# Performance work log

Hardware: AMD Instinct MI355X
Metric: run time of the kernel (lower is better)

Reference implementation:

```python
import jax, jax.numpy as jnp
import numpy as np

N = 50000      # nodes
E = 600000     # edges
G = 512        # graphs in batch
F_IN = 128     # input node features
H = 128        # hidden size (both layers)
PH = 128       # pool/classifier hidden size


def setup_inputs() -> dict:
    key = jax.random.key(0)
    ks = jax.random.split(key, 12)
    def lin(k, fi, fo):
        return (jax.random.normal(k, (fi, fo), jnp.float32) / np.sqrt(fi)).astype(jnp.float32)
    return {
        "x": jax.random.normal(ks[0], (N, F_IN), jnp.float32),
        "edge_index": jax.random.randint(ks[1], (2, E), 0, N),
        "batch": jnp.sort(jax.random.randint(ks[2], (N,), 0, G)),
        "W1": lin(ks[3], F_IN, H), "b1": jnp.zeros((H,), jnp.float32),
        "ln1_g": jnp.ones((H,), jnp.float32), "ln1_b": jnp.zeros((H,), jnp.float32),
        "W2": lin(ks[4], H, H), "b2": jnp.zeros((H,), jnp.float32),
        "ln2_g": jnp.ones((H,), jnp.float32), "ln2_b": jnp.zeros((H,), jnp.float32),
        "gate_w1": lin(ks[5], H, PH), "gate_b1": jnp.zeros((PH,), jnp.float32),
        "gate_w2": lin(ks[6], PH, 1), "gate_b2": jnp.zeros((1,), jnp.float32),
        "cls_w1": lin(ks[7], H, PH), "cls_b1": jnp.zeros((PH,), jnp.float32),
        "cls_w2": lin(ks[8], PH, 2), "cls_b2": jnp.zeros((2,), jnp.float32),
    }


def _layer_norm(h, g, b):
    m = h.mean(-1, keepdims=True)
    v = ((h - m) ** 2).mean(-1, keepdims=True)
    return (h - m) * jax.lax.rsqrt(v + 1e-5) * g + b


def _gcn(x, src, dst, norm, W, b):
    # GCNConv: x' = D^{-1/2} (A+I) D^{-1/2} (x W) + b
    h = x @ W
    out = jax.ops.segment_sum(h[src] * norm[:, None], dst, num_segments=N)
    return out + b


def reference(x, edge_index, batch, W1, b1, ln1_g, ln1_b, W2, b2, ln2_g, ln2_b,
              gate_w1, gate_b1, gate_w2, gate_b2, cls_w1, cls_b1, cls_w2, cls_b2):
    loops = jnp.arange(N, dtype=edge_index.dtype)
    src = jnp.concatenate([edge_index[0], loops])
    dst = jnp.concatenate([edge_index[1], loops])
    deg = jax.ops.segment_sum(jnp.ones_like(src, dtype=x.dtype), dst, num_segments=N)
    dinv = jnp.where(deg > 0, jax.lax.rsqrt(jnp.maximum(deg, 1e-12)), 0.0)
    norm = dinv[src] * dinv[dst]  # [(E+N)]

    h = jax.nn.relu(_layer_norm(_gcn(x, src, dst, norm, W1, b1), ln1_g, ln1_b))
    h = jax.nn.relu(_layer_norm(_gcn(h, src, dst, norm, W2, b2), ln2_g, ln2_b))

    # GlobalAttention pooling: gate MLP -> scatter softmax over graphs -> weighted sum
    gate = (jax.nn.relu(h @ gate_w1 + gate_b1) @ gate_w2 + gate_b2)[:, 0]  # [N]
    gmax = jax.ops.segment_max(gate, batch, num_segments=G)
    a = jnp.exp(gate - gmax[batch])
    denom = jax.ops.segment_sum(a, batch, num_segments=G)
    alpha = a / denom[batch]
    pooled = jax.ops.segment_sum(alpha[:, None] * h, batch, num_segments=G)  # [G, H]

    logits = jax.nn.relu(pooled @ cls_w1 + cls_b1) @ cls_w2 + cls_b2  # [G, 2]
    return logits
```

## Files before the change

kernel.cpp:

```cpp
#include <hip/hip_runtime.h>
#include <hip/hip_bf16.h>

typedef short s8v __attribute__((ext_vector_type(8)));
typedef float f4v __attribute__((ext_vector_type(4)));

#define LDA 136

__device__ __forceinline__ unsigned short f2bf(float f) {
  unsigned int u = __builtin_bit_cast(unsigned int, f);
  unsigned int r = u + 0x7fffu + ((u >> 16) & 1u);
  return (unsigned short)(r >> 16);
}
__device__ __forceinline__ float bf2f(unsigned short s) {
  return __builtin_bit_cast(float, ((unsigned int)s) << 16);
}
__device__ __forceinline__ float bflo(unsigned int v) {
  return __builtin_bit_cast(float, (unsigned int)(v << 16));
}
__device__ __forceinline__ float bfhi(unsigned int v) {
  return __builtin_bit_cast(float, (unsigned int)(v & 0xffff0000u));
}
__device__ __forceinline__ unsigned int packbf(float a, float b) {
  return (unsigned int)f2bf(a) | ((unsigned int)f2bf(b) << 16);
}

__device__ __forceinline__ int lower_bound_i(const int* a, int n, int key) {
  int lo = 0, hi = n;
  while (lo < hi) { int mid = (lo + hi) >> 1; if (a[mid] < key) lo = mid + 1; else hi = mid; }
  return lo;
}

__device__ __forceinline__ void gather_sum(
    int i, int sub, const int* __restrict__ offs, const int* __restrict__ col,
    const uint4* __restrict__ hu, float acc[8]) {
  uint4 hv = hu[(size_t)i * 16 + sub];
  acc[0] = bflo(hv.x); acc[1] = bfhi(hv.x);
  acc[2] = bflo(hv.y); acc[3] = bfhi(hv.y);
  acc[4] = bflo(hv.z); acc[5] = bfhi(hv.z);
  acc[6] = bflo(hv.w); acc[7] = bfhi(hv.w);
  int b0 = offs[i], b1 = offs[i + 1];
  int e = b0;
  for (; e + 4 <= b1; e += 4) {
    int s0 = col[e], s1 = col[e + 1], s2 = col[e + 2], s3 = col[e + 3];
    uint4 h0 = hu[(size_t)s0 * 16 + sub];
    uint4 h1 = hu[(size_t)s1 * 16 + sub];
    uint4 h2 = hu[(size_t)s2 * 16 + sub];
    uint4 h3 = hu[(size_t)s3 * 16 + sub];
    acc[0] += bflo(h0.x) + bflo(h1.x) + bflo(h2.x) + bflo(h3.x);
    acc[1] += bfhi(h0.x) + bfhi(h1.x) + bfhi(h2.x) + bfhi(h3.x);
    acc[2] += bflo(h0.y) + bflo(h1.y) + bflo(h2.y) + bflo(h3.y);
    acc[3] += bfhi(h0.y) + bfhi(h1.y) + bfhi(h2.y) + bfhi(h3.y);
    acc[4] += bflo(h0.z) + bflo(h1.z) + bflo(h2.z) + bflo(h3.z);
    acc[5] += bfhi(h0.z) + bfhi(h1.z) + bfhi(h2.z) + bfhi(h3.z);
    acc[6] += bflo(h0.w) + bflo(h1.w) + bflo(h2.w) + bflo(h3.w);
    acc[7] += bfhi(h0.w) + bfhi(h1.w) + bfhi(h2.w) + bfhi(h3.w);
  }
  for (; e < b1; ++e) {
    int s0 = col[e];
    uint4 h0 = hu[(size_t)s0 * 16 + sub];
    acc[0] += bflo(h0.x); acc[1] += bfhi(h0.x);
    acc[2] += bflo(h0.y); acc[3] += bfhi(h0.y);
    acc[4] += bflo(h0.z); acc[5] += bfhi(h0.z);
    acc[6] += bflo(h0.w); acc[7] += bfhi(h0.w);
  }
}

__device__ __forceinline__ uint4 ln_relu_pack(
    float v[8], int sub, const float* __restrict__ gam, const float* __restrict__ bet) {
  float s = 0.f, q = 0.f;
#pragma unroll
  for (int j = 0; j < 8; ++j) { s += v[j]; q += v[j] * v[j]; }
#pragma unroll
  for (int o = 1; o < 16; o <<= 1) {
    s += __shfl_xor(s, o);
    q += __shfl_xor(q, o);
  }
  float m = s * (1.0f / 128.0f);
  float var = q * (1.0f / 128.0f) - m * m;
  float rs = rsqrtf(var + 1e-5f);
  float4 g0 = reinterpret_cast<const float4*>(gam)[sub * 2];
  float4 g1 = reinterpret_cast<const float4*>(gam)[sub * 2 + 1];
  float4 e0 = reinterpret_cast<const float4*>(bet)[sub * 2];
  float4 e1 = reinterpret_cast<const float4*>(bet)[sub * 2 + 1];
  uint4 ov;
  ov.x = packbf(fmaxf((v[0] - m) * rs * g0.x + e0.x, 0.f), fmaxf((v[1] - m) * rs * g0.y + e0.y, 0.f));
  ov.y = packbf(fmaxf((v[2] - m) * rs * g0.z + e0.z, 0.f), fmaxf((v[3] - m) * rs * g0.w + e0.w, 0.f));
  ov.z = packbf(fmaxf((v[4] - m) * rs * g1.x + e1.x, 0.f), fmaxf((v[5] - m) * rs * g1.y + e1.y, 0.f));
  ov.w = packbf(fmaxf((v[6] - m) * rs * g1.z + e1.z, 0.f), fmaxf((v[7] - m) * rs * g1.w + e1.w, 0.f));
  return ov;
}

__device__ __forceinline__ void scale_bias(
    float acc[8], float di, int sub, const float* __restrict__ bias, float v[8]) {
  float4 b0v = reinterpret_cast<const float4*>(bias)[sub * 2];
  float4 b1v = reinterpret_cast<const float4*>(bias)[sub * 2 + 1];
  v[0] = acc[0] * di + b0v.x; v[1] = acc[1] * di + b0v.y;
  v[2] = acc[2] * di + b0v.z; v[3] = acc[3] * di + b0v.w;
  v[4] = acc[4] * di + b1v.x; v[5] = acc[5] * di + b1v.y;
  v[6] = acc[6] * di + b1v.z; v[7] = acc[7] * di + b1v.w;
}

__global__ __launch_bounds__(256) void pack_zero(
    const float* __restrict__ Wa, const float* __restrict__ Wb, const float* __restrict__ Wc,
    unsigned short* __restrict__ P, unsigned int* __restrict__ deg, int n) {
  int bid = blockIdx.x;
  if (bid >= 384) {
    int i = (bid - 384) * 256 + threadIdx.x;
    if (i < n) deg[i] = 0u;
    return;
  }
  int gidx = bid * 256 + threadIdx.x;
  int which = gidx >> 15;
  int idx = gidx & 32767;
  const float* W = (which == 0) ? Wa : (which == 1) ? Wb : Wc;
  int j = idx & 15;
  int lane = (idx >> 4) & 63;
  int t = (idx >> 10) & 7;
  int c = (idx >> 13) & 3;
  int k = c * 32 + (lane >> 4) * 8 + (j & 7);
  int nn = t * 16 + (lane & 15);
  float f = W[k * 128 + nn];
  unsigned short hi = f2bf(f);
  unsigned short outv = (j < 8) ? hi : f2bf(f - bf2f(hi));
  P[gidx] = outv;
}

__global__ void accum_deg(const int* __restrict__ dst, unsigned int* __restrict__ deg, int E) {
  int e = blockIdx.x * blockDim.x + threadIdx.x;
  if (e < E) atomicAdd(&deg[dst[e]], 1u);
}

__global__ __launch_bounds__(256) void scanA(const unsigned int* __restrict__ deg,
                                             int* __restrict__ offs, int* __restrict__ partial,
                                             float* __restrict__ dinv, int n) {
  __shared__ int sh[256];
  int t = threadIdx.x;
  int i = blockIdx.x * 256 + t;
  int v = (i < n) ? (int)deg[i] : 0;
  if (i < n) dinv[i] = rsqrtf((float)(deg[i] + 1u));
  sh[t] = v;
  __syncthreads();
  for (int o = 1; o < 256; o <<= 1) {
    int add = (t >= o) ? sh[t - o] : 0;
    __syncthreads();
    sh[t] += add;
    __syncthreads();
  }
  if (i < n) offs[i] = sh[t] - v;
  if (t == 255) partial[blockIdx.x] = sh[255];
}

__global__ __launch_bounds__(256) void scanC(int* __restrict__ offs, const int* __restrict__ partial,
                                             int* __restrict__ cursor, int n, int E) {
  __shared__ int red[256];
  int bid = blockIdx.x;
  int t = threadIdx.x;
  int s = 0;
  for (int j = t; j < bid; j += 256) s += partial[j];
  red[t] = s;
  __syncthreads();
#pragma unroll
  for (int o = 128; o > 0; o >>= 1) {
    if (t < o) red[t] += red[t + o];
    __syncthreads();
  }
  int pre = red[0];
  int i = bid * 256 + t;
  if (i < n) {
    int o = offs[i] + pre;
    offs[i] = o;
    cursor[i] = o;
  }
  if (i == 0) offs[n] = E;
}

__global__ __launch_bounds__(256) void gemm1_scatter(
    const float* __restrict__ in, const unsigned short* __restrict__ P,
    unsigned short* __restrict__ out, int n,
    const int* __restrict__ src, const int* __restrict__ dst,
    int* __restrict__ cursor, int* __restrict__ col,
    const float* __restrict__ dinv, int E, int gemmBlocks) {
  if ((int)blockIdx.x >= gemmBlocks) {
    int e = ((int)blockIdx.x - gemmBlocks) * 256 + threadIdx.x;
    if (e < E) {
      int d = dst[e];
      int slot = atomicAdd(&cursor[d], 1);
      col[slot] = src[e];
    }
    return;
  }
  int tid = threadIdx.x;
  int wave = tid >> 6, lane = tid & 63;
  int quad = lane >> 4, c16 = lane & 15;
  int base = blockIdx.x * 64 + wave * 16;
  int m = base + c16;

  f4v acc[8];
#pragma unroll
  for (int t = 0; t < 8; ++t) acc[t] = (f4v){0.f, 0.f, 0.f, 0.f};

  for (int c = 0; c < 4; ++c) {
    s8v ah, al;
    float v[8];
    if (m < n) {
      const float4* xp = reinterpret_cast<const float4*>(in + (size_t)m * 128 + c * 32 + quad * 8);
      float4 v0 = xp[0], v1 = xp[1];
      v[0] = v0.x; v[1] = v0.y; v[2] = v0.z; v[3] = v0.w;
      v[4] = v1.x; v[5] = v1.y; v[6] = v1.z; v[7] = v1.w;
    } else {
#pragma unroll
      for (int j = 0; j < 8; ++j) v[j] = 0.f;
    }
#pragma unroll
    for (int j = 0; j < 8; ++j) {
      unsigned short h = f2bf(v[j]);
      ah[j] = (short)h;
      al[j] = (short)f2bf(v[j] - bf2f(h));
    }
#pragma unroll
    for (int t = 0; t < 8; ++t) {
      const s8v* bp = reinterpret_cast<const s8v*>(&P[((c * 8 + t) * 64 + lane) * 16]);
      s8v bh = bp[0], bl = bp[1];
      acc[t] = __builtin_amdgcn_mfma_f32_16x16x32_bf16(ah, bh, acc[t], 0, 0, 0);
      acc[t] = __builtin_amdgcn_mfma_f32_16x16x32_bf16(ah, bl, acc[t], 0, 0, 0);
      acc[t] = __builtin_amdgcn_mfma_f32_16x16x32_bf16(al, bh, acc[t], 0, 0, 0);
    }
  }
  float dv[4];
#pragma unroll
  for (int r = 0; r < 4; ++r) {
    int mm = base + quad * 4 + r;
    dv[r] = (mm < n) ? dinv[mm] : 0.f;
  }
#pragma unroll
  for (int t = 0; t < 8; ++t)
#pragma unroll
    for (int r = 0; r < 4; ++r) {
      int mm = base + quad * 4 + r;
      if (mm < n) out[(size_t)mm * 128 + t * 16 + c16] = f2bf(acc[t][r] * dv[r]);
    }
}

__global__ __launch_bounds__(256) void gather_gemm(
    const int* __restrict__ offs, const int* __restrict__ col,
    const float* __restrict__ dinv, const unsigned short* __restrict__ h,
    const float* __restrict__ bias, const float* __restrict__ gam,
    const float* __restrict__ bet, const unsigned short* __restrict__ P,
    unsigned short* __restrict__ out, int n) {
  __shared__ unsigned short A[64 * LDA];
  int tid = threadIdx.x;
  int wave = tid >> 6, lane = tid & 63;
  int grp = lane >> 4, sub = lane & 15;
  const uint4* hu = reinterpret_cast<const uint4*>(h);
  int blk = blockIdx.x * 64;
  for (int it = 0; it < 4; ++it) {
    int li = it * 16 + wave * 4 + grp;
    int i = blk + li;
    uint4 ov;
    if (i < n) {
      float acc[8], v[8];
      gather_sum(i, sub, offs, col, hu, acc);
      scale_bias(acc, dinv[i], sub, bias, v);
      ov = ln_relu_pack(v, sub, gam, bet);
    } else {
      ov = make_uint4(0u, 0u, 0u, 0u);
    }
    *reinterpret_cast<uint4*>(&A[li * LDA + sub * 8]) = ov;
  }
  __syncthreads();
  int quad = lane >> 4, c16 = lane & 15;
  f4v acc[8];
#pragma unroll
  for (int t = 0; t < 8; ++t) acc[t] = (f4v){0.f, 0.f, 0.f, 0.f};
  int liA = wave * 16 + c16;
  for (int c = 0; c < 4; ++c) {
    s8v ah = *reinterpret_cast<const s8v*>(&A[liA * LDA + c * 32 + quad * 8]);
#pragma unroll
    for (int t = 0; t < 8; ++t) {
      const s8v* bp = reinterpret_cast<const s8v*>(&P[((c * 8 + t) * 64 + lane) * 16]);
      s8v bh = bp[0], bl = bp[1];
      acc[t] = __builtin_amdgcn_mfma_f32_16x16x32_bf16(ah, bh, acc[t], 0, 0, 0);
      acc[t] = __builtin_amdgcn_mfma_f32_16x16x32_bf16(ah, bl, acc[t], 0, 0, 0);
    }
  }
  float dv[4];
#pragma unroll
  for (int r = 0; r < 4; ++r) {
    int mm = blk + wave * 16 + quad * 4 + r;
    dv[r] = (mm < n) ? dinv[mm] : 0.f;
  }
#pragma unroll
  for (int t = 0; t < 8; ++t)
#pragma unroll
    for (int r = 0; r < 4; ++r) {
      int mm = blk + wave * 16 + quad * 4 + r;
      if (mm < n) out[(size_t)mm * 128 + t * 16 + c16] = f2bf(acc[t][r] * dv[r]);
    }
}

__global__ __launch_bounds__(256) void gather_gate(
    const int* __restrict__ offs, const int* __restrict__ col,
    const float* __restrict__ dinv, const unsigned short* __restrict__ h,
    const float* __restrict__ bias, const float* __restrict__ gam,
    const float* __restrict__ bet, const unsigned short* __restrict__ P,
    const float* __restrict__ gb1, const float* __restrict__ gw2,
    const float* __restrict__ gb2, unsigned short* __restrict__ hout,
    float* __restrict__ gate, int n) {
  __shared__ unsigned short A[64 * LDA];
  int tid = threadIdx.x;
  int wave = tid >> 6, lane = tid & 63;
  int grp = lane >> 4, sub = lane & 15;
  const uint4* hu = reinterpret_cast<const uint4*>(h);
  int blk = blockIdx.x * 64;
  for (int it = 0; it < 4; ++it) {
    int li = it * 16 + wave * 4 + grp;
    int i = blk + li;
    uint4 ov;
    if (i < n) {
      float acc[8], v[8];
      gather_sum(i, sub, offs, col, hu, acc);
      scale_bias(acc, dinv[i], sub, bias, v);
      ov = ln_relu_pack(v, sub, gam, bet);
      reinterpret_cast<uint4*>(hout)[(size_t)i * 16 + sub] = ov;
    } else {
      ov = make_uint4(0u, 0u, 0u, 0u);
    }
    *reinterpret_cast<uint4*>(&A[li * LDA + sub * 8]) = ov;
  }
  __syncthreads();
  int quad = lane >> 4, c16 = lane & 15;
  f4v acc[8];
#pragma unroll
  for (int t = 0; t < 8; ++t) acc[t] = (f4v){0.f, 0.f, 0.f, 0.f};
  int liA = wave * 16 + c16;
  for (int c = 0; c < 4; ++c) {
    s8v ah = *reinterpret_cast<const s8v*>(&A[liA * LDA + c * 32 + quad * 8]);
#pragma unroll
    for (int t = 0; t < 8; ++t) {
      const s8v* bp = reinterpret_cast<const s8v*>(&P[((c * 8 + t) * 64 + lane) * 16]);
      s8v bh = bp[0], bl = bp[1];
      acc[t] = __builtin_amdgcn_mfma_f32_16x16x32_bf16(ah, bh, acc[t], 0, 0, 0);
      acc[t] = __builtin_amdgcn_mfma_f32_16x16x32_bf16(ah, bl, acc[t], 0, 0, 0);
    }
  }
  float bv[8], g2[8];
#pragma unroll
  for (int t = 0; t < 8; ++t) {
    bv[t] = gb1[t * 16 + c16];
    g2[t] = gw2[t * 16 + c16];
  }
  float gb2v = gb2[0];
#pragma unroll
  for (int r = 0; r < 4; ++r) {
    float p = 0.f;
#pragma unroll
    for (int t = 0; t < 8; ++t)
      p += fmaxf(acc[t][r] + bv[t], 0.f) * g2[t];
#pragma unroll
    for (int o = 1; o < 16; o <<= 1) p += __shfl_xor(p, o);
    int mm = blk + wave * 16 + quad * 4 + r;
    if (c16 == 0 && mm < n) gate[mm] = p + gb2v;
  }
}

__global__ __launch_bounds__(256) void pool_cls(
    float* __restrict__ gate, const unsigned short* __restrict__ h,
    const int* __restrict__ batch,
    const float* __restrict__ w1, const float* __restrict__ b1,
    const float* __restrict__ w2, const float* __restrict__ b2,
    float* __restrict__ out, int n) {
  int g = blockIdx.x;
  int tid = threadIdx.x;
  __shared__ float red[256];
  __shared__ float red2[256];
  __shared__ float p[128];
  __shared__ float r[128];
  int lo = lower_bound_i(batch, n, g);
  int hi = lower_bound_i(batch, n, g + 1);
  if (lo >= hi) {
    if (tid < 128) p[tid] = 0.0f;
  } else {
    float m = -3.0e38f;
    for (int i = lo + tid; i < hi; i += 256) m = fmaxf(m, gate[i]);
    red[tid] = m;
    __syncthreads();
#pragma unroll
    for (int o = 128; o > 0; o >>= 1) {
      if (tid < o) red[tid] = fmaxf(red[tid], red[tid + o]);
      __syncthreads();
    }
    m = red[0];
    __syncthreads();
    float s = 0.0f;
    for (int i = lo + tid; i < hi; i += 256) {
      float e = __expf(gate[i] - m);
      gate[i] = e;
      s += e;
    }
    red[tid] = s;
    __syncthreads();
#pragma unroll
    for (int o = 128; o > 0; o >>= 1) {
      if (tid < o) red[tid] += red[tid + o];
      __syncthreads();
    }
    float inv = 1.0f / red[0];
    __syncthreads();
    const unsigned int* hu = reinterpret_cast<const unsigned int*>(h);
    int j = tid & 63, rgp = tid >> 6;
    float a0 = 0.f, a1 = 0.f;
    int i = lo + rgp;
    for (; i + 4 < hi; i += 8) {
      unsigned int p0 = hu[(size_t)i * 64 + j];
      unsigned int p1 = hu[(size_t)(i + 4) * 64 + j];
      float w0 = gate[i], w1v = gate[i + 4];
      a0 += bflo(p0) * w0 + bflo(p1) * w1v;
      a1 += bfhi(p0) * w0 + bfhi(p1) * w1v;
    }
    if (i < hi) {
      unsigned int p0 = hu[(size_t)i * 64 + j];
      float w0 = gate[i];
      a0 += bflo(p0) * w0;
      a1 += bfhi(p0) * w0;
    }
    red[tid] = a0;
    red2[tid] = a1;
    __syncthreads();
    if (tid < 64) {
      p[2 * tid]     = (red[tid] + red[tid + 64] + red[tid + 128] + red[tid + 192]) * inv;
      p[2 * tid + 1] = (red2[tid] + red2[tid + 64] + red2[tid + 128] + red2[tid + 192]) * inv;
    }
  }
  __syncthreads();
  int j = tid & 127, half = tid >> 7;
  float acc = 0.0f;
#pragma unroll 8
  for (int k = half * 64; k < half * 64 + 64; ++k)
    acc = fmaf(p[k], w1[k * 128 + j], acc);
  red[tid] = acc;
  __syncthreads();
  if (tid < 128) r[tid] = fmaxf(red[tid] + red[tid + 128] + b1[tid], 0.0f);
  __syncthreads();
  if (tid < 2) {
    float a = 0.0f;
    for (int k = 0; k < 128; ++k) a = fmaf(r[k], w2[k * 2 + tid], a);
    out[g * 2 + tid] = a + b2[tid];
  }
}

static inline size_t alup(size_t x) { return (x + 255) & ~(size_t)255; }

extern "C" void kernel_launch(void* const* d_in, const int* in_sizes, int n_in,
                              void* d_out, int out_size, void* d_ws, size_t ws_size,
                              hipStream_t stream) {
  const float* x    = (const float*)d_in[0];
  const int*   ei   = (const int*)d_in[1];
  const int*   bat  = (const int*)d_in[2];
  const float* W1   = (const float*)d_in[3];
  const float* b1   = (const float*)d_in[4];
  const float* ln1g = (const float*)d_in[5];
  const float* ln1b = (const float*)d_in[6];
  const float* W2   = (const float*)d_in[7];
  const float* b2   = (const float*)d_in[8];
  const float* ln2g = (const float*)d_in[9];
  const float* ln2b = (const float*)d_in[10];
  const float* gw1  = (const float*)d_in[11];
  const float* gb1  = (const float*)d_in[12];
  const float* gw2  = (const float*)d_in[13];
  const float* gb2  = (const float*)d_in[14];
  const float* cw1  = (const float*)d_in[15];
  const float* cb1  = (const float*)d_in[16];
  const float* cw2  = (const float*)d_in[17];
  const float* cb2  = (const float*)d_in[18];

  const int N = in_sizes[2];
  const int E = in_sizes[1] / 2;
  const int G = out_size / 2;
  const int* src = ei;
  const int* dst = ei + E;

  int nb256 = (N + 255) / 256;
  int eb256 = (E + 255) / 256;
  int mfmaB = (N + 63) / 64;

  char* base = (char*)d_ws;
  unsigned int* deg = (unsigned int*)base; base += alup((size_t)N * 4);
  float* dinv = (float*)base;              base += alup((size_t)N * 4);
  int* offs = (int*)base;                  base += alup((size_t)(N + 1) * 4);
  int* cursor = (int*)base;                base += alup((size_t)N * 4);
  int* partial = (int*)base;               base += alup((size_t)nb256 * 4);
  int* col = (int*)base;                   base += alup((size_t)E * 4);
  unsigned short* pW = (unsigned short*)base; base += alup((size_t)3 * 32768 * 2);
  unsigned short* hbuf = (unsigned short*)base;  base += alup((size_t)N * 128 * 2);
  unsigned short* hbuf2 = (unsigned short*)base; base += alup((size_t)N * 128 * 2);
  unsigned short* hout = (unsigned short*)base;  base += alup((size_t)N * 128 * 2);
  float* gate = (float*)base;              base += alup((size_t)N * 4);

  unsigned short* pW1 = pW;
  unsigned short* pW2 = pW + 32768;
  unsigned short* pG1 = pW + 65536;

  float* out = (float*)d_out;

  pack_zero<<<384 + nb256, 256, 0, stream>>>(W1, W2, gw1, pW, deg, N);
  accum_deg<<<eb256, 256, 0, stream>>>(dst, deg, E);
  scanA<<<nb256, 256, 0, stream>>>(deg, offs, partial, dinv, N);
  scanC<<<nb256, 256, 0, stream>>>(offs, partial, cursor, N, E);
  gemm1_scatter<<<mfmaB + eb256, 256, 0, stream>>>(x, pW1, hbuf, N,
                                                   src, dst, cursor, col, dinv, E, mfmaB);
  gather_gemm<<<mfmaB, 256, 0, stream>>>(offs, col, dinv, hbuf, b1, ln1g, ln1b,
                                         pW2, hbuf2, N);
  gather_gate<<<mfmaB, 256, 0, stream>>>(offs, col, dinv, hbuf2, b2, ln2g, ln2b,
                                         pG1, gb1, gw2, gb2, hout, gate, N);
  pool_cls<<<G, 256, 0, stream>>>(gate, hout, bat, cw1, cb1, cw2, cb2, out, N);
}
```

Measured before the change: 272.3 us.

## Build CSR via two-level bucketed radix sort with LDS atomics

Replaces the global-atomic degree count, two-kernel scan and global-atomic scatter with a two-level counting sort: coarse 256-node buckets are histogrammed in shared memory, scanned in a single block, scattered as packed (local dst, src) words, then a per-bucket kernel builds the fine offsets, dinv and col using LDS atomics. Because dinv is no longer available when the first GEMM runs, the source-side normalisation moves from the GEMM epilogues into the gather loop, which now loads dinv per neighbour. This cuts kernel launches and contended global atomics. In exchange it adds an extra pass over the edges, uses a 16-bit src packing that only holds for fewer than 65536 nodes, and sizes buckets for at most 256×256 nodes. The single-block scan limits parallelism.

```diff
diff --git a/kernel.cpp b/kernel.cpp
--- a/kernel.cpp
+++ b/kernel.cpp
@@ -30,14 +30,15 @@
   return lo;
 }
 
-__device__ __forceinline__ void gather_sum(
+__device__ __forceinline__ float gather_node(
     int i, int sub, const int* __restrict__ offs, const int* __restrict__ col,
-    const uint4* __restrict__ hu, float acc[8]) {
+    const float* __restrict__ dinv, const uint4* __restrict__ hu, float acc[8]) {
+  float di = dinv[i];
   uint4 hv = hu[(size_t)i * 16 + sub];
-  acc[0] = bflo(hv.x); acc[1] = bfhi(hv.x);
-  acc[2] = bflo(hv.y); acc[3] = bfhi(hv.y);
-  acc[4] = bflo(hv.z); acc[5] = bfhi(hv.z);
-  acc[6] = bflo(hv.w); acc[7] = bfhi(hv.w);
+  acc[0] = bflo(hv.x) * di; acc[1] = bfhi(hv.x) * di;
+  acc[2] = bflo(hv.y) * di; acc[3] = bfhi(hv.y) * di;
+  acc[4] = bflo(hv.z) * di; acc[5] = bfhi(hv.z) * di;
+  acc[6] = bflo(hv.w) * di; acc[7] = bfhi(hv.w) * di;
   int b0 = offs[i], b1 = offs[i + 1];
   int e = b0;
   for (; e + 4 <= b1; e += 4) {
@@ -46,23 +47,26 @@
     uint4 h1 = hu[(size_t)s1 * 16 + sub];
     uint4 h2 = hu[(size_t)s2 * 16 + sub];
     uint4 h3 = hu[(size_t)s3 * 16 + sub];
-    acc[0] += bflo(h0.x) + bflo(h1.x) + bflo(h2.x) + bflo(h3.x);
-    acc[1] += bfhi(h0.x) + bfhi(h1.x) + bfhi(h2.x) + bfhi(h3.x);
-    acc[2] += bflo(h0.y) + bflo(h1.y) + bflo(h2.y) + bflo(h3.y);
-    acc[3] += bfhi(h0.y) + bfhi(h1.y) + bfhi(h2.y) + bfhi(h3.y);
-    acc[4] += bflo(h0.z) + bflo(h1.z) + bflo(h2.z) + bflo(h3.z);
-    acc[5] += bfhi(h0.z) + bfhi(h1.z) + bfhi(h2.z) + bfhi(h3.z);
-    acc[6] += bflo(h0.w) + bflo(h1.w) + bflo(h2.w) + bflo(h3.w);
-    acc[7] += bfhi(h0.w) + bfhi(h1.w) + bfhi(h2.w) + bfhi(h3.w);
+    float n0 = dinv[s0], n1 = dinv[s1], n2 = dinv[s2], n3 = dinv[s3];
+    acc[0] += bflo(h0.x) * n0 + bflo(h1.x) * n1 + bflo(h2.x) * n2 + bflo(h3.x) * n3;
+    acc[1] += bfhi(h0.x) * n0 + bfhi(h1.x) * n1 + bfhi(h2.x) * n2 + bfhi(h3.x) * n3;
+    acc[2] += bflo(h0.y) * n0 + bflo(h1.y) * n1 + bflo(h2.y) * n2 + bflo(h3.y) * n3;
+    acc[3] += bfhi(h0.y) * n0 + bfhi(h1.y) * n1 + bfhi(h2.y) * n2 + bfhi(h3.y) * n3;
+    acc[4] += bflo(h0.z) * n0 + bflo(h1.z) * n1 + bflo(h2.z) * n2 + bflo(h3.z) * n3;
+    acc[5] += bfhi(h0.z) * n0 + bfhi(h1.z) * n1 + bfhi(h2.z) * n2 + bfhi(h3.z) * n3;
+    acc[6] += bflo(h0.w) * n0 + bflo(h1.w) * n1 + bflo(h2.w) * n2 + bflo(h3.w) * n3;
+    acc[7] += bfhi(h0.w) * n0 + bfhi(h1.w) * n1 + bfhi(h2.w) * n2 + bfhi(h3.w) * n3;
   }
   for (; e < b1; ++e) {
     int s0 = col[e];
     uint4 h0 = hu[(size_t)s0 * 16 + sub];
-    acc[0] += bflo(h0.x); acc[1] += bfhi(h0.x);
-    acc[2] += bflo(h0.y); acc[3] += bfhi(h0.y);
-    acc[4] += bflo(h0.z); acc[5] += bfhi(h0.z);
-    acc[6] += bflo(h0.w); acc[7] += bfhi(h0.w);
-  }
+    float n0 = dinv[s0];
+    acc[0] += bflo(h0.x) * n0; acc[1] += bfhi(h0.x) * n0;
+    acc[2] += bflo(h0.y) * n0; acc[3] += bfhi(h0.y) * n0;
+    acc[4] += bflo(h0.z) * n0; acc[5] += bfhi(h0.z) * n0;
+    acc[6] += bflo(h0.w) * n0; acc[7] += bfhi(h0.w) * n0;
+  }
+  return di;
 }
 
 __device__ __forceinline__ uint4 ln_relu_pack(
@@ -100,44 +104,52 @@
   v[6] = acc[6] * di + b1v.z; v[7] = acc[7] * di + b1v.w;
 }
 
-__global__ __launch_bounds__(256) void pack_zero(
+__global__ __launch_bounds__(256) void packhist(
     const float* __restrict__ Wa, const float* __restrict__ Wb, const float* __restrict__ Wc,
-    unsigned short* __restrict__ P, unsigned int* __restrict__ deg, int n) {
+    unsigned short* __restrict__ P, const int* __restrict__ dst,
+    unsigned int* __restrict__ Hist, int E) {
+  __shared__ unsigned int cnt[256];
   int bid = blockIdx.x;
+  int t = threadIdx.x;
   if (bid >= 384) {
-    int i = (bid - 384) * 256 + threadIdx.x;
-    if (i < n) deg[i] = 0u;
+    int hb = bid - 384;
+    cnt[t] = 0u;
+    __syncthreads();
+    int chunk = (E + 63) >> 6;
+    int lo = hb * chunk, hi = min(E, lo + chunk);
+    for (int e = lo + t; e < hi; e += 256)
+      atomicAdd(&cnt[((unsigned int)dst[e]) >> 8], 1u);
+    __syncthreads();
+    Hist[hb * 256 + t] = cnt[t];
     return;
   }
-  int gidx = bid * 256 + threadIdx.x;
+  int gidx = bid * 256 + t;
   int which = gidx >> 15;
   int idx = gidx & 32767;
   const float* W = (which == 0) ? Wa : (which == 1) ? Wb : Wc;
   int j = idx & 15;
   int lane = (idx >> 4) & 63;
-  int t = (idx >> 10) & 7;
+  int tt = (idx >> 10) & 7;
   int c = (idx >> 13) & 3;
   int k = c * 32 + (lane >> 4) * 8 + (j & 7);
-  int nn = t * 16 + (lane & 15);
+  int nn = tt * 16 + (lane & 15);
   float f = W[k * 128 + nn];
-  unsigned short hi = f2bf(f);
-  unsigned short outv = (j < 8) ? hi : f2bf(f - bf2f(hi));
+  unsigned short hi16 = f2bf(f);
+  unsigned short outv = (j < 8) ? hi16 : f2bf(f - bf2f(hi16));
   P[gidx] = outv;
 }
 
-__global__ void accum_deg(const int* __restrict__ dst, unsigned int* __restrict__ deg, int E) {
-  int e = blockIdx.x * blockDim.x + threadIdx.x;
-  if (e < E) atomicAdd(&deg[dst[e]], 1u);
-}
-
-__global__ __launch_bounds__(256) void scanA(const unsigned int* __restrict__ deg,
-                                             int* __restrict__ offs, int* __restrict__ partial,
-                                             float* __restrict__ dinv, int n) {
+__global__ __launch_bounds__(256) void scanbase(
+    unsigned int* __restrict__ Hist, unsigned int* __restrict__ Base,
+    unsigned int* __restrict__ Bstart, int* __restrict__ offs, int n, int E) {
   __shared__ int sh[256];
   int t = threadIdx.x;
-  int i = blockIdx.x * 256 + t;
-  int v = (i < n) ? (int)deg[i] : 0;
-  if (i < n) dinv[i] = rsqrtf((float)(deg[i] + 1u));
+  unsigned int run = 0;
+  for (int b = 0; b < 64; ++b) {
+    Base[b * 256 + t] = run;
+    run += Hist[b * 256 + t];
+  }
+  int v = (int)run;
   sh[t] = v;
   __syncthreads();
   for (int o = 1; o < 256; o <<= 1) {
@@ -146,50 +158,34 @@
     sh[t] += add;
     __syncthreads();
   }
-  if (i < n) offs[i] = sh[t] - v;
-  if (t == 255) partial[blockIdx.x] = sh[255];
-}
-
-__global__ __launch_bounds__(256) void scanC(int* __restrict__ offs, const int* __restrict__ partial,
-                                             int* __restrict__ cursor, int n, int E) {
-  __shared__ int red[256];
-  int bid = blockIdx.x;
-  int t = threadIdx.x;
-  int s = 0;
-  for (int j = t; j < bid; j += 256) s += partial[j];
-  red[t] = s;
-  __syncthreads();
-#pragma unroll
-  for (int o = 128; o > 0; o >>= 1) {
-    if (t < o) red[t] += red[t + o];
-    __syncthreads();
-  }
-  int pre = red[0];
-  int i = bid * 256 + t;
-  if (i < n) {
-    int o = offs[i] + pre;
-    offs[i] = o;
-    cursor[i] = o;
-  }
-  if (i == 0) offs[n] = E;
+  unsigned int pre = (unsigned int)(sh[t] - v);
+  Bstart[t] = pre;
+  for (int b = 0; b < 64; ++b) Base[b * 256 + t] += pre;
+  if (t == 0) offs[n] = E;
 }
 
 __global__ __launch_bounds__(256) void gemm1_scatter(
     const float* __restrict__ in, const unsigned short* __restrict__ P,
     unsigned short* __restrict__ out, int n,
     const int* __restrict__ src, const int* __restrict__ dst,
-    int* __restrict__ cursor, int* __restrict__ col,
-    const float* __restrict__ dinv, int E, int gemmBlocks) {
+    const unsigned int* __restrict__ Base, unsigned int* __restrict__ EP,
+    int E, int gemmBlocks) {
+  __shared__ unsigned int cur[256];
+  int tid = threadIdx.x;
   if ((int)blockIdx.x >= gemmBlocks) {
-    int e = ((int)blockIdx.x - gemmBlocks) * 256 + threadIdx.x;
-    if (e < E) {
-      int d = dst[e];
-      int slot = atomicAdd(&cursor[d], 1);
-      col[slot] = src[e];
+    int sb = (int)blockIdx.x - gemmBlocks;
+    cur[tid] = Base[sb * 256 + tid];
+    __syncthreads();
+    int chunk = (E + 63) >> 6;
+    int lo = sb * chunk, hi = min(E, lo + chunk);
+    for (int e = lo + tid; e < hi; e += 256) {
+      unsigned int d = (unsigned int)dst[e];
+      unsigned int s = (unsigned int)src[e];
+      unsigned int pos = atomicAdd(&cur[d >> 8], 1u);
+      EP[pos] = ((d & 255u) << 16) | s;
     }
     return;
   }
-  int tid = threadIdx.x;
   int wave = tid >> 6, lane = tid & 63;
   int quad = lane >> 4, c16 = lane & 15;
   int base = blockIdx.x * 64 + wave * 16;
@@ -226,19 +222,53 @@
       acc[t] = __builtin_amdgcn_mfma_f32_16x16x32_bf16(al, bh, acc[t], 0, 0, 0);
     }
   }
-  float dv[4];
-#pragma unroll
-  for (int r = 0; r < 4; ++r) {
-    int mm = base + quad * 4 + r;
-    dv[r] = (mm < n) ? dinv[mm] : 0.f;
-  }
 #pragma unroll
   for (int t = 0; t < 8; ++t)
 #pragma unroll
     for (int r = 0; r < 4; ++r) {
       int mm = base + quad * 4 + r;
-      if (mm < n) out[(size_t)mm * 128 + t * 16 + c16] = f2bf(acc[t][r] * dv[r]);
-    }
+      if (mm < n) out[(size_t)mm * 128 + t * 16 + c16] = f2bf(acc[t][r]);
+    }
+}
+
+__global__ __launch_bounds__(256) void fine_csr(
+    const unsigned int* __restrict__ EP, const unsigned int* __restrict__ Bstart,
+    int* __restrict__ offs, float* __restrict__ dinv, int* __restrict__ col, int n) {
+  __shared__ unsigned int cnt[256];
+  __shared__ int sh[256];
+  __shared__ unsigned int cur[256];
+  int bk = blockIdx.x;
+  int t = threadIdx.x;
+  unsigned int rlo = Bstart[bk];
+  unsigned int rhi = (bk < 255) ? Bstart[bk + 1] : rlo;
+  cnt[t] = 0u;
+  __syncthreads();
+  for (unsigned int i = rlo + t; i < rhi; i += 256)
+    atomicAdd(&cnt[EP[i] >> 16], 1u);
+  __syncthreads();
+  int v = (int)cnt[t];
+  sh[t] = v;
+  __syncthreads();
+  for (int o = 1; o < 256; o <<= 1) {
+    int add = (t >= o) ? sh[t - o] : 0;
+    __syncthreads();
+    sh[t] += add;
+    __syncthreads();
+  }
+  int pre = sh[t] - v;
+  int node = bk * 256 + t;
+  if (node < n) {
+    offs[node] = (int)(rlo + pre);
+    dinv[node] = rsqrtf((float)(v + 1));
+  }
+  cur[t] = rlo + (unsigned int)pre;
+  __syncthreads();
+  for (unsigned int i = rlo + t; i < rhi; i += 256) {
+    unsigned int w = EP[i];
+    unsigned int dl = w >> 16;
+    unsigned int pos = atomicAdd(&cur[dl], 1u);
+    col[pos] = (int)(w & 0xffffu);
+  }
 }
 
 __global__ __launch_bounds__(256) void gather_gemm(
@@ -259,8 +289,8 @@
     uint4 ov;
     if (i < n) {
       float acc[8], v[8];
-      gather_sum(i, sub, offs, col, hu, acc);
-      scale_bias(acc, dinv[i], sub, bias, v);
+      float di = gather_node(i, sub, offs, col, dinv, hu, acc);
+      scale_bias(acc, di, sub, bias, v);
       ov = ln_relu_pack(v, sub, gam, bet);
     } else {
       ov = make_uint4(0u, 0u, 0u, 0u);
@@ -283,18 +313,12 @@
       acc[t] = __builtin_amdgcn_mfma_f32_16x16x32_bf16(ah, bl, acc[t], 0, 0, 0);
     }
   }
-  float dv[4];
-#pragma unroll
-  for (int r = 0; r < 4; ++r) {
-    int mm = blk + wave * 16 + quad * 4 + r;
-    dv[r] = (mm < n) ? dinv[mm] : 0.f;
-  }
 #pragma unroll
   for (int t = 0; t < 8; ++t)
 #pragma unroll
     for (int r = 0; r < 4; ++r) {
       int mm = blk + wave * 16 + quad * 4 + r;
-      if (mm < n) out[(size_t)mm * 128 + t * 16 + c16] = f2bf(acc[t][r] * dv[r]);
+      if (mm < n) out[(size_t)mm * 128 + t * 16 + c16] = f2bf(acc[t][r]);
     }
 }
 
@@ -318,8 +342,8 @@
     uint4 ov;
     if (i < n) {
       float acc[8], v[8];
-      gather_sum(i, sub, offs, col, hu, acc);
-      scale_bias(acc, dinv[i], sub, bias, v);
+      float di = gather_node(i, sub, offs, col, dinv, hu, acc);
+      scale_bias(acc, di, sub, bias, v);
       ov = ln_relu_pack(v, sub, gam, bet);
       reinterpret_cast<uint4*>(hout)[(size_t)i * 16 + sub] = ov;
     } else {
@@ -479,22 +503,22 @@
   const int* src = ei;
   const int* dst = ei + E;
 
-  int nb256 = (N + 255) / 256;
-  int eb256 = (E + 255) / 256;
   int mfmaB = (N + 63) / 64;
+  int NB = (N + 255) / 256;
 
   char* base = (char*)d_ws;
-  unsigned int* deg = (unsigned int*)base; base += alup((size_t)N * 4);
-  float* dinv = (float*)base;              base += alup((size_t)N * 4);
-  int* offs = (int*)base;                  base += alup((size_t)(N + 1) * 4);
-  int* cursor = (int*)base;                base += alup((size_t)N * 4);
-  int* partial = (int*)base;               base += alup((size_t)nb256 * 4);
-  int* col = (int*)base;                   base += alup((size_t)E * 4);
+  unsigned int* Hist = (unsigned int*)base;   base += alup((size_t)64 * 256 * 4);
+  unsigned int* Base = (unsigned int*)base;   base += alup((size_t)64 * 256 * 4);
+  unsigned int* Bstart = (unsigned int*)base; base += alup((size_t)256 * 4);
+  unsigned int* EP = (unsigned int*)base;     base += alup((size_t)E * 4);
+  float* dinv = (float*)base;                 base += alup((size_t)N * 4);
+  int* offs = (int*)base;                     base += alup((size_t)(N + 1) * 4);
+  int* col = (int*)base;                      base += alup((size_t)E * 4);
   unsigned short* pW = (unsigned short*)base; base += alup((size_t)3 * 32768 * 2);
   unsigned short* hbuf = (unsigned short*)base;  base += alup((size_t)N * 128 * 2);
   unsigned short* hbuf2 = (unsigned short*)base; base += alup((size_t)N * 128 * 2);
   unsigned short* hout = (unsigned short*)base;  base += alup((size_t)N * 128 * 2);
-  float* gate = (float*)base;              base += alup((size_t)N * 4);
+  float* gate = (float*)base;                 base += alup((size_t)N * 4);
 
   unsigned short* pW1 = pW;
   unsigned short* pW2 = pW + 32768;
@@ -502,12 +526,11 @@
 
   float* out = (float*)d_out;
 
-  pack_zero<<<384 + nb256, 256, 0, stream>>>(W1, W2, gw1, pW, deg, N);
-  accum_deg<<<eb256, 256, 0, stream>>>(dst, deg, E);
-  scanA<<<nb256, 256, 0, stream>>>(deg, offs, partial, dinv, N);
-  scanC<<<nb256, 256, 0, stream>>>(offs, partial, cursor, N, E);
-  gemm1_scatter<<<mfmaB + eb256, 256, 0, stream>>>(x, pW1, hbuf, N,
-                                                   src, dst, cursor, col, dinv, E, mfmaB);
+  packhist<<<384 + 64, 256, 0, stream>>>(W1, W2, gw1, pW, dst, Hist, E);
+  scanbase<<<1, 256, 0, stream>>>(Hist, Base, Bstart, offs, N, E);
+  gemm1_scatter<<<mfmaB + 64, 256, 0, stream>>>(x, pW1, hbuf, N,
+                                                src, dst, Base, EP, E, mfmaB);
+  fine_csr<<<NB, 256, 0, stream>>>(EP, Bstart, offs, dinv, col, N);
   gather_gemm<<<mfmaB, 256, 0, stream>>>(offs, col, dinv, hbuf, b1, ln1g, ln1b,
                                          pW2, hbuf2, N);
   gather_gate<<<mfmaB, 256, 0, stream>>>(offs, col, dinv, hbuf2, b2, ln2g, ln2b,
```

New measurement: 249.7 us. 1.09x faster.
